# Kernel optimization log

Measured on AMD Instinct MI355X. Metric: run time of the kernel, lower is better.

The kernel has to match this reference:

```python
import jax, jax.numpy as jnp
import numpy as np

D_MODEL = 1024
NUM_HEADS = 16
HEAD_DIM = D_MODEL // NUM_HEADS


def setup_inputs() -> dict:
    key = jax.random.key(0)
    k_x, k_qkv, k_o = jax.random.split(key, 3)
    B, L = 2, 2048
    x = jax.random.normal(k_x, (B, L, D_MODEL), dtype=jnp.float32)
    # torch Linear weight [out, in]; y = x @ W.T. Scale ~ kaiming-uniform-ish.
    s = 1.0 / np.sqrt(D_MODEL)
    W_qkv = jax.random.uniform(k_qkv, (3 * D_MODEL, D_MODEL), dtype=jnp.float32, minval=-s, maxval=s)
    W_o = jax.random.uniform(k_o, (D_MODEL, D_MODEL), dtype=jnp.float32, minval=-s, maxval=s)
    return {"x": x, "W_qkv": W_qkv, "W_o": W_o}


def reference(x, W_qkv, W_o):
    B, L, D = x.shape
    H, dk = NUM_HEADS, HEAD_DIM
    qkv = (x @ W_qkv.T).reshape(B, L, 3, H, dk)
    q = qkv[:, :, 0].transpose(0, 2, 1, 3)  # [B,H,L,dk]
    k = qkv[:, :, 1].transpose(0, 2, 1, 3)
    v = qkv[:, :, 2].transpose(0, 2, 1, 3)
    scale = 1.0 / np.sqrt(dk).astype(np.float32)
    attn = jnp.einsum('bhqd,bhkd->bhqk', q, k) * scale  # [B,H,L,L]
    causal = jnp.tril(jnp.ones((L, L), dtype=bool))
    attn = jnp.where(causal, attn, -jnp.inf)
    attn = jax.nn.softmax(attn, axis=-1)
    y = jnp.einsum('bhqk,bhkd->bhqd', attn, v)  # [B,H,L,dk]
    y = y.transpose(0, 2, 1, 3).reshape(B, L, D)
    return y @ W_o.T
```

## Files before the change

### kernel.cpp

```cpp
#include <hip/hip_runtime.h>

typedef unsigned short u16;
typedef unsigned int   u32;

typedef __attribute__((ext_vector_type(4))) float  f32x4;
typedef __attribute__((ext_vector_type(8))) __bf16 bf16x8;

#define B_  2
#define L_  2048
#define H_  16

__device__ static inline u16 f2bf(float f) {
  u32 u = __builtin_bit_cast(u32, f);
  u32 r = u + 0x7fffu + ((u >> 16) & 1u);
  return (u16)(r >> 16);
}
__device__ static inline u32 pack2(float a, float b) {
  return (u32)f2bf(a) | ((u32)f2bf(b) << 16);
}

__device__ static inline void gload_lds16(const u16* g, u16* lds) {
  __builtin_amdgcn_global_load_lds((__attribute__((address_space(1))) void*)(g),
                                   (__attribute__((address_space(3))) void*)(lds),
                                   16, 0, 0);
}

__global__ __launch_bounds__(256) void cvt3_kernel(
    const float4* __restrict__ a, uint2* __restrict__ ao, int na,
    const float4* __restrict__ b, uint2* __restrict__ bo, int nb,
    const float4* __restrict__ c, uint2* __restrict__ co, int nc)
{
  const int step = gridDim.x * 256;
  for (int i = blockIdx.x * 256 + threadIdx.x; i < na; i += step) {
    float4 f = a[i];
    ao[i] = make_uint2(pack2(f.x, f.y), pack2(f.z, f.w));
  }
  for (int i = blockIdx.x * 256 + threadIdx.x; i < nb; i += step) {
    float4 f = b[i];
    bo[i] = make_uint2(pack2(f.x, f.y), pack2(f.z, f.w));
  }
  for (int i = blockIdx.x * 256 + threadIdx.x; i < nc; i += step) {
    float4 f = c[i];
    co[i] = make_uint2(pack2(f.x, f.y), pack2(f.z, f.w));
  }
}

template <bool OUT_F32>
__global__ __launch_bounds__(256) void gemm_bt_kernel(
    const u16* __restrict__ A, const u16* __restrict__ Bt, void* __restrict__ Cv,
    const int K, const int N)
{
  __shared__ __attribute__((aligned(16))) u16 Al[128 * 64];
  __shared__ __attribute__((aligned(16))) u16 Bl[128 * 64];

  const int tid  = threadIdx.x;
  const int w    = tid >> 6;
  const int lane = tid & 63;
  const int m0 = blockIdx.y * 128;
  const int n0 = blockIdx.x * 128;
  const int mo = (w >> 1) * 64;
  const int no = (w & 1) * 64;

  const int srow = w * 32 + (lane >> 3);
  const int scol = (((lane & 7) ^ ((lane >> 3) & 7)) * 8);

  const f32x4 zero = {0.f, 0.f, 0.f, 0.f};
  f32x4 acc[4][4];
  #pragma unroll
  for (int i = 0; i < 4; ++i)
    #pragma unroll
    for (int j = 0; j < 4; ++j) acc[i][j] = zero;

  const int frow = lane & 15;
  const int fg   = lane >> 4;

  for (int k0 = 0; k0 < K; k0 += 64) {
    __syncthreads();
    #pragma unroll
    for (int inst = 0; inst < 4; ++inst) {
      const int r = srow + inst * 8;
      gload_lds16(A  + (size_t)(m0 + r) * K + k0 + scol, &Al[(w * 32 + inst * 8) * 64]);
      gload_lds16(Bt + (size_t)(n0 + r) * K + k0 + scol, &Bl[(w * 32 + inst * 8) * 64]);
    }
    __syncthreads();
    #pragma unroll
    for (int ks = 0; ks < 2; ++ks) {
      const int fco = ((ks * 4 + fg) ^ (frow & 7)) * 8;
      bf16x8 af[4], bfr[4];
      #pragma unroll
      for (int i = 0; i < 4; ++i)
        af[i] = *(const bf16x8*)&Al[(mo + i * 16 + frow) * 64 + fco];
      #pragma unroll
      for (int j = 0; j < 4; ++j)
        bfr[j] = *(const bf16x8*)&Bl[(no + j * 16 + frow) * 64 + fco];
      #pragma unroll
      for (int i = 0; i < 4; ++i)
        #pragma unroll
        for (int j = 0; j < 4; ++j)
          acc[i][j] = __builtin_amdgcn_mfma_f32_16x16x32_bf16(af[i], bfr[j], acc[i][j], 0, 0, 0);
    }
  }

  const int crow0 = m0 + mo + (lane >> 4) * 4;
  const int ccol0 = n0 + no + (lane & 15);
  #pragma unroll
  for (int i = 0; i < 4; ++i)
    #pragma unroll
    for (int j = 0; j < 4; ++j)
      #pragma unroll
      for (int r = 0; r < 4; ++r) {
        const size_t idx = (size_t)(crow0 + i * 16 + r) * N + (ccol0 + j * 16);
        if (OUT_F32) ((float*)Cv)[idx] = acc[i][j][r];
        else         ((u16*)Cv)[idx]   = f2bf(acc[i][j][r]);
      }
}

__global__ __launch_bounds__(512) void attn_mfma_kernel(const u16* __restrict__ qkv,
                                                        u16* __restrict__ y)
{
  __shared__ __attribute__((aligned(16))) unsigned char smem[81920];

  const int tid  = threadIdx.x;
  const int g    = tid >> 8;
  const int w    = (tid >> 6) & 3;
  const int lane = tid & 63;
  const int fr   = lane & 15;
  const int fg   = lane >> 4;
  const int bh   = blockIdx.x;
  const int pi   = blockIdx.y;
  const int bb   = bh >> 4;
  const int hh   = bh & 15;
  const size_t rb = (size_t)bb * L_;

  u16* Kt   = (u16*)(smem + g * 40960);
  u32* Vtd  = (u32*)(smem + g * 40960 + 16384);
  u32* PTd  = (u32*)(smem + g * 40960 + 32768) + w * 512;
  float* Ocmb = (float*)(smem + 40960);
  float* Lcmb = (float*)(smem + 40960 + 17408);

  const int kkp = lane & 31;
  const int dc  = 2 * w + (lane >> 5);

  const int ksr = w * 16 + (lane >> 3);
  const int ksc = (((lane & 7) ^ ((lane >> 3) & 7)) * 8);
  const int kco0 = ((fg) ^ (fr & 7)) * 8;
  const int kco1 = ((4 + fg) ^ (fr & 7)) * 8;

  const int cro0 = 4 * ((fg) ^ (fr & 7));
  const int cro1 = 4 * ((4 + fg) ^ (fr & 7));
  const int pwo  = 4 * (fr & 7);

  const f32x4 zero = {0.f, 0.f, 0.f, 0.f};

  for (int pass = 0; pass < 2; ++pass) {
    const int qt = pass ? (31 - pi) : pi;
    const int q0 = qt * 64;
    const int qw = q0 + w * 16;
    const int n  = qt + 1;
    const int c0 = (n + 1) >> 1;
    const int myCnt  = g ? (n - c0) : c0;
    const int myBase = g ? c0 : 0;
    const int phases = c0;

    const bf16x8 qf0 = *(const bf16x8*)(qkv + (rb + qw + fr) * 3072 + hh * 64 + fg * 8);
    const bf16x8 qf1 = *(const bf16x8*)(qkv + (rb + qw + fr) * 3072 + hh * 64 + 32 + fg * 8);

    f32x4 oacc[4];
    #pragma unroll
    for (int mt = 0; mt < 4; ++mt) oacc[mt] = zero;
    float lsum = 0.f;

    __syncthreads();
    if (myCnt > 0) {
      const int kt = myBase * 64;
      #pragma unroll
      for (int inst = 0; inst < 2; ++inst)
        gload_lds16(qkv + (rb + kt + ksr + inst * 8) * 3072 + 1024 + hh * 64 + ksc,
                    &Kt[(w * 16 + inst * 8) * 64]);
      const u16* vp = qkv + (rb + kt + 2 * kkp) * 3072 + 2048 + hh * 64 + dc * 8;
      uint4 va = *(const uint4*)vp;
      uint4 vb = *(const uint4*)(vp + 3072);
      u16 a16[8], b16[8];
      *(uint4*)a16 = va; *(uint4*)b16 = vb;
      #pragma unroll
      for (int i = 0; i < 8; ++i)
        Vtd[(dc * 8 + i) * 32 + 4 * ((kkp >> 2) ^ i) + (kkp & 3)] =
            (u32)a16[i] | ((u32)b16[i] << 16);
    }

    int cur = 0;
    for (int it = 0; it < phases; ++it) {
      __syncthreads();

      const int  kt       = (myBase + it) * 64;
      const bool active   = it < myCnt;
      const bool havenext = (it + 1) < myCnt;
      uint4 va, vb;
      if (havenext) {
        #pragma unroll
        for (int inst = 0; inst < 2; ++inst)
          gload_lds16(qkv + (rb + kt + 64 + ksr + inst * 8) * 3072 + 1024 + hh * 64 + ksc,
                      &Kt[(cur ^ 1) * 4096 + (w * 16 + inst * 8) * 64]);
        const u16* vp = qkv + (rb + kt + 64 + 2 * kkp) * 3072 + 2048 + hh * 64 + dc * 8;
        va = *(const uint4*)vp;
        vb = *(const uint4*)(vp + 3072);
      }

      if (active) {
        f32x4 sacc[4];
        #pragma unroll
        for (int nt = 0; nt < 4; ++nt) sacc[nt] = zero;
        #pragma unroll
        for (int nt = 0; nt < 4; ++nt) {
          bf16x8 kf0 = *(const bf16x8*)&Kt[cur * 4096 + (nt * 16 + fr) * 64 + kco0];
          sacc[nt] = __builtin_amdgcn_mfma_f32_16x16x32_bf16(kf0, qf0, sacc[nt], 0, 0, 0);
          bf16x8 kf1 = *(const bf16x8*)&Kt[cur * 4096 + (nt * 16 + fr) * 64 + kco1];
          sacc[nt] = __builtin_amdgcn_mfma_f32_16x16x32_bf16(kf1, qf1, sacc[nt], 0, 0, 0);
        }

        if (kt == q0) {
          #pragma unroll
          for (int nt = 0; nt < 4; ++nt) {
            float p[4];
            #pragma unroll
            for (int r = 0; r < 4; ++r) {
              p[r] = (nt * 16 + 4 * fg + r > w * 16 + fr)
                         ? 0.f : __expf(sacc[nt][r] * 0.125f);
              lsum += p[r];
            }
            *(uint2*)&PTd[fr * 32 + ((8 * nt + 2 * fg) ^ pwo)] =
                make_uint2(pack2(p[0], p[1]), pack2(p[2], p[3]));
          }
        } else {
          #pragma unroll
          for (int nt = 0; nt < 4; ++nt) {
            float p[4];
            #pragma unroll
            for (int r = 0; r < 4; ++r) {
              p[r] = __expf(sacc[nt][r] * 0.125f);
              lsum += p[r];
            }
            *(uint2*)&PTd[fr * 32 + ((8 * nt + 2 * fg) ^ pwo)] =
                make_uint2(pack2(p[0], p[1]), pack2(p[2], p[3]));
          }
        }

        #pragma unroll
        for (int ks = 0; ks < 2; ++ks) {
          bf16x8 pf = *(const bf16x8*)&PTd[fr * 32 + (ks ? cro1 : cro0)];
          #pragma unroll
          for (int mt = 0; mt < 4; ++mt) {
            bf16x8 vf = *(const bf16x8*)&Vtd[cur * 2048 + (mt * 16 + fr) * 32 + (ks ? cro1 : cro0)];
            oacc[mt] = __builtin_amdgcn_mfma_f32_16x16x32_bf16(vf, pf, oacc[mt], 0, 0, 0);
          }
        }
      }

      if (havenext) {
        u16 a16[8], b16[8];
        *(uint4*)a16 = va; *(uint4*)b16 = vb;
        #pragma unroll
        for (int i = 0; i < 8; ++i)
          Vtd[(cur ^ 1) * 2048 + (dc * 8 + i) * 32 + 4 * ((kkp >> 2) ^ i) + (kkp & 3)] =
              (u32)a16[i] | ((u32)b16[i] << 16);
      }
      cur ^= 1;
    }

    lsum += __shfl_xor(lsum, 16);
    lsum += __shfl_xor(lsum, 32);

    __syncthreads();
    if (g == 1) {
      #pragma unroll
      for (int mt = 0; mt < 4; ++mt)
        *(f32x4*)&Ocmb[(w * 16 + fr) * 68 + mt * 16 + 4 * fg] = oacc[mt];
      if (fg == 0) Lcmb[w * 16 + fr] = lsum;
    }
    __syncthreads();
    if (g == 0) {
      const float inv = 1.f / (lsum + Lcmb[w * 16 + fr]);
      u16* yp = y + (rb + qw + fr) * 1024 + hh * 64 + 4 * fg;
      #pragma unroll
      for (int mt = 0; mt < 4; ++mt) {
        f32x4 o = oacc[mt] + *(const f32x4*)&Ocmb[(w * 16 + fr) * 68 + mt * 16 + 4 * fg];
        *(uint2*)(yp + mt * 16) = make_uint2(pack2(o[0] * inv, o[1] * inv),
                                             pack2(o[2] * inv, o[3] * inv));
      }
    }
  }
}

extern "C" void kernel_launch(void* const* d_in, const int* in_sizes, int n_in,
                              void* d_out, int out_size, void* d_ws, size_t ws_size,
                              hipStream_t stream)
{
  const float* x    = (const float*)d_in[0];
  const float* Wqkv = (const float*)d_in[1];
  const float* Wo   = (const float*)d_in[2];
  float* out = (float*)d_out;

  u16* xb    = (u16*)d_ws;
  u16* Wqkvb = xb    + (size_t)4096 * 1024;
  u16* Wob   = Wqkvb + (size_t)3072 * 1024;
  u16* qkv   = Wob   + (size_t)1024 * 1024;
  u16* y     = qkv   + (size_t)4096 * 3072;

  cvt3_kernel<<<dim3(2048), dim3(256), 0, stream>>>(
      (const float4*)x,    (uint2*)xb,    4096 * 1024 / 4,
      (const float4*)Wqkv, (uint2*)Wqkvb, 3072 * 1024 / 4,
      (const float4*)Wo,   (uint2*)Wob,   1024 * 1024 / 4);

  gemm_bt_kernel<false><<<dim3(3072 / 128, 4096 / 128), dim3(256), 0, stream>>>(
      xb, Wqkvb, qkv, 1024, 3072);
  attn_mfma_kernel<<<dim3(B_ * H_, 16), dim3(512), 0, stream>>>(qkv, y);
  gemm_bt_kernel<true><<<dim3(1024 / 128, 4096 / 128), dim3(256), 0, stream>>>(
      y, Wob, out, 1024, 1024);
}
```

Baseline: 180.2 us.

## Double-buffer output GEMM with narrower tiles and truncate softmax probabilities to bf16

The GEMM kernel is templated on N-tile width and LDS double buffering. The output projection now uses 128x64 tiles, which doubles its block count and improves occupancy, and prefetches the next K-slice while computing the current one. In attention, the round-to-nearest bf16 packing of softmax probabilities is replaced by a single byte-permute truncation, cutting ALU work but adding slight rounding bias. The double-buffered path keeps one barrier per iteration and relies on the next iteration's barrier to order the async LDS loads.

```diff
diff --git a/kernel.cpp b/kernel.cpp
--- a/kernel.cpp
+++ b/kernel.cpp
@@ -17,6 +17,10 @@
 }
 __device__ static inline u32 pack2(float a, float b) {
   return (u32)f2bf(a) | ((u32)f2bf(b) << 16);
+}
+__device__ static inline u32 pack2t(float a, float b) {
+  return __builtin_amdgcn_perm(__builtin_bit_cast(u32, b),
+                               __builtin_bit_cast(u32, a), 0x07060302u);
 }
 
 __device__ static inline void gload_lds16(const u16* g, u16* lds) {
@@ -45,60 +49,78 @@
   }
 }
 
-template <bool OUT_F32>
+template <bool OUT_F32, int NT, bool DBUF>
 __global__ __launch_bounds__(256) void gemm_bt_kernel(
     const u16* __restrict__ A, const u16* __restrict__ Bt, void* __restrict__ Cv,
     const int K, const int N)
 {
-  __shared__ __attribute__((aligned(16))) u16 Al[128 * 64];
-  __shared__ __attribute__((aligned(16))) u16 Bl[128 * 64];
+  constexpr int NB = DBUF ? 2 : 1;
+  constexpr int JT = NT / 32;
+  __shared__ __attribute__((aligned(16))) u16 Al[NB][128 * 64];
+  __shared__ __attribute__((aligned(16))) u16 Bl[NB][NT * 64];
 
   const int tid  = threadIdx.x;
   const int w    = tid >> 6;
   const int lane = tid & 63;
   const int m0 = blockIdx.y * 128;
-  const int n0 = blockIdx.x * 128;
+  const int n0 = blockIdx.x * NT;
   const int mo = (w >> 1) * 64;
-  const int no = (w & 1) * 64;
-
-  const int srow = w * 32 + (lane >> 3);
+  const int no = (w & 1) * (NT / 2);
+
+  const int sr8  = lane >> 3;
   const int scol = (((lane & 7) ^ ((lane >> 3) & 7)) * 8);
 
   const f32x4 zero = {0.f, 0.f, 0.f, 0.f};
-  f32x4 acc[4][4];
+  f32x4 acc[4][JT];
   #pragma unroll
   for (int i = 0; i < 4; ++i)
     #pragma unroll
-    for (int j = 0; j < 4; ++j) acc[i][j] = zero;
+    for (int j = 0; j < JT; ++j) acc[i][j] = zero;
 
   const int frow = lane & 15;
   const int fg   = lane >> 4;
 
+  auto stage = [&](int buf, int k0) {
+    #pragma unroll
+    for (int inst = 0; inst < 4; ++inst) {
+      const int r = w * 32 + inst * 8 + sr8;
+      gload_lds16(A + (size_t)(m0 + r) * K + k0 + scol, &Al[buf][(w * 32 + inst * 8) * 64]);
+    }
+    #pragma unroll
+    for (int inst = 0; inst < NT / 32; ++inst) {
+      const int r = w * (NT / 4) + inst * 8 + sr8;
+      gload_lds16(Bt + (size_t)(n0 + r) * K + k0 + scol, &Bl[buf][(w * (NT / 4) + inst * 8) * 64]);
+    }
+  };
+
+  if (DBUF) stage(0, 0);
+
+  int cur = 0;
   for (int k0 = 0; k0 < K; k0 += 64) {
     __syncthreads();
-    #pragma unroll
-    for (int inst = 0; inst < 4; ++inst) {
-      const int r = srow + inst * 8;
-      gload_lds16(A  + (size_t)(m0 + r) * K + k0 + scol, &Al[(w * 32 + inst * 8) * 64]);
-      gload_lds16(Bt + (size_t)(n0 + r) * K + k0 + scol, &Bl[(w * 32 + inst * 8) * 64]);
-    }
-    __syncthreads();
+    if (DBUF) {
+      if (k0 + 64 < K) stage(cur ^ 1, k0 + 64);
+    } else {
+      stage(0, k0);
+      __syncthreads();
+    }
     #pragma unroll
     for (int ks = 0; ks < 2; ++ks) {
       const int fco = ((ks * 4 + fg) ^ (frow & 7)) * 8;
-      bf16x8 af[4], bfr[4];
+      bf16x8 af[4], bfr[JT];
       #pragma unroll
       for (int i = 0; i < 4; ++i)
-        af[i] = *(const bf16x8*)&Al[(mo + i * 16 + frow) * 64 + fco];
-      #pragma unroll
-      for (int j = 0; j < 4; ++j)
-        bfr[j] = *(const bf16x8*)&Bl[(no + j * 16 + frow) * 64 + fco];
+        af[i] = *(const bf16x8*)&Al[cur][(mo + i * 16 + frow) * 64 + fco];
+      #pragma unroll
+      for (int j = 0; j < JT; ++j)
+        bfr[j] = *(const bf16x8*)&Bl[cur][(no + j * 16 + frow) * 64 + fco];
       #pragma unroll
       for (int i = 0; i < 4; ++i)
         #pragma unroll
-        for (int j = 0; j < 4; ++j)
+        for (int j = 0; j < JT; ++j)
           acc[i][j] = __builtin_amdgcn_mfma_f32_16x16x32_bf16(af[i], bfr[j], acc[i][j], 0, 0, 0);
     }
+    if (DBUF) cur ^= 1;
   }
 
   const int crow0 = m0 + mo + (lane >> 4) * 4;
@@ -106,7 +128,7 @@
   #pragma unroll
   for (int i = 0; i < 4; ++i)
     #pragma unroll
-    for (int j = 0; j < 4; ++j)
+    for (int j = 0; j < JT; ++j)
       #pragma unroll
       for (int r = 0; r < 4; ++r) {
         const size_t idx = (size_t)(crow0 + i * 16 + r) * N + (ccol0 + j * 16);
@@ -229,7 +251,7 @@
               lsum += p[r];
             }
             *(uint2*)&PTd[fr * 32 + ((8 * nt + 2 * fg) ^ pwo)] =
-                make_uint2(pack2(p[0], p[1]), pack2(p[2], p[3]));
+                make_uint2(pack2t(p[0], p[1]), pack2t(p[2], p[3]));
           }
         } else {
           #pragma unroll
@@ -241,7 +263,7 @@
               lsum += p[r];
             }
             *(uint2*)&PTd[fr * 32 + ((8 * nt + 2 * fg) ^ pwo)] =
-                make_uint2(pack2(p[0], p[1]), pack2(p[2], p[3]));
+                make_uint2(pack2t(p[0], p[1]), pack2t(p[2], p[3]));
           }
         }
 
@@ -311,9 +333,9 @@
       (const float4*)Wqkv, (uint2*)Wqkvb, 3072 * 1024 / 4,
       (const float4*)Wo,   (uint2*)Wob,   1024 * 1024 / 4);
 
-  gemm_bt_kernel<false><<<dim3(3072 / 128, 4096 / 128), dim3(256), 0, stream>>>(
+  gemm_bt_kernel<false, 128, false><<<dim3(3072 / 128, 4096 / 128), dim3(256), 0, stream>>>(
       xb, Wqkvb, qkv, 1024, 3072);
   attn_mfma_kernel<<<dim3(B_ * H_, 16), dim3(512), 0, stream>>>(qkv, y);
-  gemm_bt_kernel<true><<<dim3(1024 / 128, 4096 / 128), dim3(256), 0, stream>>>(
+  gemm_bt_kernel<true, 64, true><<<dim3(1024 / 64, 4096 / 128), dim3(256), 0, stream>>>(
       y, Wob, out, 1024, 1024);
 }
```

New measurement: 165.3 us. 1.09x faster.
